# Kernel tuning notes

Measured on AMD Instinct MI355X. Metric: run time of the kernel, lower is better.

## Reference

```python
import jax, jax.numpy as jnp
import numpy as np

N = 100000
E = 1600000
IN_C = 128
OUT_C = 8
HEADS = 8
EDGE_DIM = 4
ACTUAL_OUT = OUT_C * HEADS  # 64, concat=True
BN_EPS = 1e-5
NEG_SLOPE = 0.2  # PyG GATConv default leaky_relu slope


def setup_inputs() -> dict:
    key = jax.random.key(0)
    ks = jax.random.split(key, 12)
    s = lambda fan_in: 1.0 / np.sqrt(fan_in)
    return {
        "x": jax.random.normal(ks[0], (N, IN_C), jnp.float32),
        "edge_index": jax.random.randint(ks[1], (2, E), 0, N, jnp.int64),
        "edge_attr": jax.random.normal(ks[2], (E, EDGE_DIM), jnp.float32),
        # GATConv params
        "W": jax.random.normal(ks[3], (IN_C, HEADS * OUT_C), jnp.float32) * s(IN_C),
        "att_src": jax.random.normal(ks[4], (HEADS, OUT_C), jnp.float32) * s(OUT_C),
        "att_dst": jax.random.normal(ks[5], (HEADS, OUT_C), jnp.float32) * s(OUT_C),
        "W_edge": jax.random.normal(ks[6], (EDGE_DIM, HEADS * OUT_C), jnp.float32) * s(EDGE_DIM),
        "att_edge": jax.random.normal(ks[7], (HEADS, OUT_C), jnp.float32) * s(OUT_C),
        "bias": jnp.zeros((HEADS * OUT_C,), jnp.float32),
        # BatchNorm params
        "bn_w": jnp.ones((ACTUAL_OUT,), jnp.float32),
        "bn_b": jnp.zeros((ACTUAL_OUT,), jnp.float32),
        # residual Linear (in_channels != heads*out_channels)
        "res_W": jax.random.normal(ks[8], (IN_C, ACTUAL_OUT), jnp.float32) * s(IN_C),
        "res_b": jnp.zeros((ACTUAL_OUT,), jnp.float32),
    }


def reference(x, edge_index, edge_attr, W, att_src, att_dst, W_edge, att_edge,
              bias, bn_w, bn_b, res_W, res_b):
    src, dst = edge_index[0], edge_index[1]
    n = x.shape[0]

    # --- GATConv (PyG semantics, eval mode: dropout is identity) ---
    h = (x @ W).reshape(n, HEADS, OUT_C)                       # [N,H,C]
    a_src = jnp.einsum('nhc,hc->nh', h, att_src)               # [N,H]
    a_dst = jnp.einsum('nhc,hc->nh', h, att_dst)               # [N,H]
    he = (edge_attr @ W_edge).reshape(-1, HEADS, OUT_C)        # [E,H,C]
    a_edge = jnp.einsum('ehc,hc->eh', he, att_edge)            # [E,H]

    logits = jax.nn.leaky_relu(a_src[src] + a_dst[dst] + a_edge, NEG_SLOPE)  # [E,H]
    # segment softmax over edges grouped by destination node
    m = jax.ops.segment_max(logits, dst, num_segments=n)       # [N,H]
    m = jnp.where(jnp.isfinite(m), m, 0.0)
    num = jnp.exp(logits - jax.lax.stop_gradient(m)[dst])      # [E,H]
    denom = jax.ops.segment_sum(num, dst, num_segments=n)      # [N,H]
    alpha = num / (denom[dst] + 1e-16)                         # [E,H]

    msg = alpha[:, :, None] * h[src]                           # [E,H,C]
    out = jax.ops.segment_sum(msg, dst, num_segments=n)        # [N,H,C]
    out = out.reshape(n, HEADS * OUT_C) + bias                 # concat heads

    # --- BatchNorm (training-mode batch stats, biased variance) ---
    mean = out.mean(axis=0)
    var = out.var(axis=0)
    out = (out - mean) * jax.lax.rsqrt(var + BN_EPS) * bn_w + bn_b

    # --- ELU, (dropout=identity in eval), residual ---
    out = jax.nn.elu(out)
    identity = x @ res_W + res_b
    return out + identity
```

## Files before the change

kernel.cpp:

```cpp
#include <hip/hip_runtime.h>
#include <hip/hip_bf16.h>

#define N_NODES 100000
#define N_EDGES 1600000

typedef unsigned short ushort_t;

__device__ __forceinline__ float rlane(float v, int l) {
    return __int_as_float(__builtin_amdgcn_readlane(__float_as_int(v), l));
}
__device__ __forceinline__ ushort_t f2bf(float f) {
    unsigned u = __float_as_uint(f);
    u += 0x7FFFu + ((u >> 16) & 1u);
    return (ushort_t)(u >> 16);
}
__device__ __forceinline__ float bf2f(ushort_t b) {
    return __uint_as_float((unsigned)b << 16);
}
__device__ __forceinline__ void atomic_pk_add_bf16(ushort_t* addr, unsigned packed) {
    asm volatile("global_atomic_pk_add_bf16 %0, %1, off sc1"
                 :: "v"(addr), "v"(packed) : "memory");
}

__global__ __launch_bounds__(256) void k1_node(
    const float* __restrict__ x, const float* __restrict__ W,
    const float* __restrict__ resW, const float* __restrict__ att_src,
    const float* __restrict__ att_dst, const float* __restrict__ res_b,
    ushort_t* __restrict__ h, float* __restrict__ ident,
    float* __restrict__ a_src, float* __restrict__ a_dst)
{
    __shared__ float wl[128 * 128];
    const int tid = threadIdx.x;
    for (int i = tid; i < 8192; i += 256) {
        int k = i >> 6, j = i & 63;
        wl[k * 128 + j] = W[i];
        wl[k * 128 + 64 + j] = resW[i];
    }
    __syncthreads();

    const int lane = tid & 63;
    const int wid = tid >> 6;
    const float asv = att_src[lane];
    const float adv = att_dst[lane];
    const float rbv = res_b[lane];

    for (int g = 0; g < 4; ++g) {
        const int nbase = blockIdx.x * 128 + g * 32 + wid * 8;
        float xlo[8], xhi[8], ah[8], ai[8];
        #pragma unroll
        for (int r = 0; r < 8; ++r) {
            const int n = nbase + r;
            if (n < N_NODES) {
                xlo[r] = x[(size_t)n * 128 + lane];
                xhi[r] = x[(size_t)n * 128 + 64 + lane];
            } else { xlo[r] = 0.f; xhi[r] = 0.f; }
            ah[r] = 0.f; ai[r] = 0.f;
        }
        #pragma unroll 4
        for (int k = 0; k < 64; ++k) {
            const float w0 = wl[k * 128 + lane];
            const float w1 = wl[k * 128 + 64 + lane];
            #pragma unroll
            for (int r = 0; r < 8; ++r) {
                const float xv = rlane(xlo[r], k);
                ah[r] = fmaf(w0, xv, ah[r]);
                ai[r] = fmaf(w1, xv, ai[r]);
            }
        }
        #pragma unroll 4
        for (int k = 64; k < 128; ++k) {
            const float w0 = wl[k * 128 + lane];
            const float w1 = wl[k * 128 + 64 + lane];
            #pragma unroll
            for (int r = 0; r < 8; ++r) {
                const float xv = rlane(xhi[r], k - 64);
                ah[r] = fmaf(w0, xv, ah[r]);
                ai[r] = fmaf(w1, xv, ai[r]);
            }
        }
        #pragma unroll
        for (int r = 0; r < 8; ++r) {
            const int n = nbase + r;
            float ps = ah[r] * asv;
            float pd = ah[r] * adv;
            ps += __shfl_xor(ps, 1); ps += __shfl_xor(ps, 2); ps += __shfl_xor(ps, 4);
            pd += __shfl_xor(pd, 1); pd += __shfl_xor(pd, 2); pd += __shfl_xor(pd, 4);
            if (n < N_NODES) {
                h[(size_t)n * 64 + lane] = f2bf(ah[r]);
                ident[(size_t)n * 64 + lane] = ai[r] + rbv;
                if ((lane & 7) == 0) {
                    a_src[n * 8 + (lane >> 3)] = ps;
                    a_dst[n * 8 + (lane >> 3)] = pd;
                }
            }
        }
    }
}

__global__ __launch_bounds__(256) void k2_edge(
    const int* __restrict__ ei, const float* __restrict__ ea,
    const ushort_t* __restrict__ h, const float* __restrict__ a_src,
    const float* __restrict__ a_dst, const float* __restrict__ W_edge,
    const float* __restrict__ att_edge,
    float* __restrict__ denom, ushort_t* __restrict__ out_raw)
{
    const int lane = threadIdx.x & 63;
    const int hd = lane >> 3;
    float ae0 = 0.f, ae1 = 0.f, ae2 = 0.f, ae3 = 0.f;
    #pragma unroll
    for (int c2 = 0; c2 < 8; ++c2) {
        const float a = att_edge[hd * 8 + c2];
        ae0 = fmaf(W_edge[0 * 64 + hd * 8 + c2], a, ae0);
        ae1 = fmaf(W_edge[1 * 64 + hd * 8 + c2], a, ae1);
        ae2 = fmaf(W_edge[2 * 64 + hd * 8 + c2], a, ae2);
        ae3 = fmaf(W_edge[3 * 64 + hd * 8 + c2], a, ae3);
    }

    const int gwave = blockIdx.x * 4 + (threadIdx.x >> 6);
    const int nwave = gridDim.x * 4;
    for (int base = gwave * 64; base < N_EDGES; base += nwave * 64) {
        const int vsrc = ei[base + lane];
        const int vdst = ei[N_EDGES + base + lane];
        const float4 vea = *reinterpret_cast<const float4*>(ea + (size_t)(base + lane) * 4);
        for (int g = 0; g < 64; g += 8) {
            int s[8], d[8];
            float e0[8], e1[8], e2[8], e3[8];
            #pragma unroll
            for (int j = 0; j < 8; ++j) {
                s[j] = __builtin_amdgcn_readlane(vsrc, g + j);
                d[j] = __builtin_amdgcn_readlane(vdst, g + j);
                e0[j] = rlane(vea.x, g + j);
                e1[j] = rlane(vea.y, g + j);
                e2[j] = rlane(vea.z, g + j);
                e3[j] = rlane(vea.w, g + j);
            }
            float hv[8], as8[8], ad8[8];
            #pragma unroll
            for (int j = 0; j < 8; ++j) {
                hv[j]  = bf2f(h[(size_t)s[j] * 64 + lane]);
                as8[j] = a_src[s[j] * 8 + hd];
                ad8[j] = a_dst[d[j] * 8 + hd];
            }
            #pragma unroll
            for (int j = 0; j < 8; ++j) {
                float logit = as8[j] + ad8[j]
                            + e0[j] * ae0 + e1[j] * ae1 + e2[j] * ae2 + e3[j] * ae3;
                logit = logit > 0.f ? logit : 0.2f * logit;
                const float num = __expf(logit);
                const float v = num * hv[j];
                const float vn = __shfl_xor(v, 1);
                if ((lane & 1) == 0) {
                    const unsigned packed = (unsigned)f2bf(v) | ((unsigned)f2bf(vn) << 16);
                    atomic_pk_add_bf16(out_raw + (size_t)d[j] * 64 + lane, packed);
                }
                if ((lane & 7) == 0) atomicAdd(&denom[d[j] * 8 + hd], num);
            }
        }
    }
    asm volatile("s_waitcnt vmcnt(0)" ::: "memory");
}

__global__ __launch_bounds__(256) void k3_stats(
    const ushort_t* __restrict__ out_raw, const float* __restrict__ denom,
    const float* __restrict__ bias,
    float* __restrict__ bn_acc )
{
    const int tid = threadIdx.x;
    const int c = tid & 63;
    const float b = bias[c];
    float s1 = 0.f, s2 = 0.f;
    const int stride = gridDim.x * 4;
    for (int n = blockIdx.x * 4 + (tid >> 6); n < N_NODES; n += stride) {
        const float v = bf2f(out_raw[(size_t)n * 64 + c])
                        / (denom[n * 8 + (c >> 3)] + 1e-16f) + b;
        s1 += v; s2 += v * v;
    }
    __shared__ float r1[256], r2[256];
    r1[tid] = s1; r2[tid] = s2;
    __syncthreads();
    if (tid < 64) {
        s1 = r1[tid] + r1[tid + 64] + r1[tid + 128] + r1[tid + 192];
        s2 = r2[tid] + r2[tid + 64] + r2[tid + 128] + r2[tid + 192];
        atomicAdd(&bn_acc[c], s1);
        atomicAdd(&bn_acc[64 + c], s2);
    }
}

__global__ __launch_bounds__(256) void k4_final(
    float* __restrict__ out, const ushort_t* __restrict__ out_raw,
    const float* __restrict__ denom, const float* __restrict__ bias,
    const float* __restrict__ bn_acc, const float* __restrict__ bn_w,
    const float* __restrict__ bn_b)
{
    const int tid = threadIdx.x;
    const int c = tid & 63;
    const float b = bias[c];
    const float inv_n = 1.0f / (float)N_NODES;
    const float mean = bn_acc[c] * inv_n;
    const float var = bn_acc[64 + c] * inv_n - mean * mean;
    const float sc = bn_w[c] * rsqrtf(var + 1e-5f);
    const float sh = bn_b[c] - mean * sc;
    const int stride = gridDim.x * 4;
    for (int n = blockIdx.x * 4 + (tid >> 6); n < N_NODES; n += stride) {
        float v = bf2f(out_raw[(size_t)n * 64 + c])
                  / (denom[n * 8 + (c >> 3)] + 1e-16f) + b;
        v = v * sc + sh;
        v = v > 0.f ? v : __expf(v) - 1.f;
        out[(size_t)n * 64 + c] = v + out[(size_t)n * 64 + c];
    }
}

extern "C" void kernel_launch(void* const* d_in, const int* in_sizes, int n_in,
                              void* d_out, int out_size, void* d_ws, size_t ws_size,
                              hipStream_t stream) {
    const float* x        = (const float*)d_in[0];
    const int*   ei       = (const int*)  d_in[1];
    const float* ea       = (const float*)d_in[2];
    const float* W        = (const float*)d_in[3];
    const float* att_src  = (const float*)d_in[4];
    const float* att_dst  = (const float*)d_in[5];
    const float* W_edge   = (const float*)d_in[6];
    const float* att_edge = (const float*)d_in[7];
    const float* bias     = (const float*)d_in[8];
    const float* bn_w     = (const float*)d_in[9];
    const float* bn_b     = (const float*)d_in[10];
    const float* res_W    = (const float*)d_in[11];
    const float* res_b    = (const float*)d_in[12];

    char* ws = (char*)d_ws;
    size_t off = 0;
    ushort_t* h   = (ushort_t*)(ws + off); off += (size_t)N_NODES * 64 * 2;
    float* a_src  = (float*)(ws + off); off += (size_t)N_NODES * 8 * 4;
    float* a_dst  = (float*)(ws + off); off += (size_t)N_NODES * 8 * 4;
    char*  zstart = ws + off;
    float* denom  = (float*)(ws + off); off += (size_t)N_NODES * 8 * 4;
    ushort_t* o_raw = (ushort_t*)(ws + off); off += (size_t)N_NODES * 64 * 2;
    float* bn_acc = (float*)(ws + off); off += 128 * 4;
    size_t zbytes = (size_t)((ws + off) - zstart);

    float* ident = (float*)d_out;

    (void)hipMemsetAsync(zstart, 0, zbytes, stream);
    k1_node<<<(N_NODES + 127) / 128, 256, 0, stream>>>(
        x, W, res_W, att_src, att_dst, res_b, h, ident, a_src, a_dst);
    k2_edge<<<6250, 256, 0, stream>>>(ei, ea, h, a_src, a_dst, W_edge, att_edge,
                                      denom, o_raw);
    k3_stats<<<2048, 256, 0, stream>>>(o_raw, denom, bias, bn_acc);
    k4_final<<<2048, 256, 0, stream>>>((float*)d_out, o_raw, denom, bias,
                                       bn_acc, bn_w, bn_b);
}
```

Baseline: 553.3 us.

## Compute node projection and residual GEMM with bf16 MFMA instructions

Replaces the scalar FMA/readlane node GEMM with a bf16 MFMA 16x16x32 kernel. Weight fragments are kept in registers and each wave processes 32-row tiles in a persistent grid-stride loop over 512 blocks. The aim is to shrink the time spent on the dense x@W and x@res_W products. In exchange, x and the weights are rounded to bf16, which lowers the precision of h, the attention logits and the residual identity.

Result: faster. 484.3 us (-12.5%).

```diff
diff --git a/kernel.cpp b/kernel.cpp
--- a/kernel.cpp
+++ b/kernel.cpp
@@ -5,6 +5,8 @@
 #define N_EDGES 1600000
 
 typedef unsigned short ushort_t;
+typedef __attribute__((ext_vector_type(4))) float f32x4;
+typedef __attribute__((ext_vector_type(8))) short bf16x8v;
 
 __device__ __forceinline__ float rlane(float v, int l) {
     return __int_as_float(__builtin_amdgcn_readlane(__float_as_int(v), l));
@@ -22,75 +24,98 @@
                  :: "v"(addr), "v"(packed) : "memory");
 }
 
-__global__ __launch_bounds__(256) void k1_node(
+__global__ __launch_bounds__(256) void k1_mfma(
     const float* __restrict__ x, const float* __restrict__ W,
     const float* __restrict__ resW, const float* __restrict__ att_src,
     const float* __restrict__ att_dst, const float* __restrict__ res_b,
     ushort_t* __restrict__ h, float* __restrict__ ident,
     float* __restrict__ a_src, float* __restrict__ a_dst)
 {
-    __shared__ float wl[128 * 128];
-    const int tid = threadIdx.x;
-    for (int i = tid; i < 8192; i += 256) {
-        int k = i >> 6, j = i & 63;
-        wl[k * 128 + j] = W[i];
-        wl[k * 128 + 64 + j] = resW[i];
-    }
-    __syncthreads();
-
-    const int lane = tid & 63;
-    const int wid = tid >> 6;
-    const float asv = att_src[lane];
-    const float adv = att_dst[lane];
-    const float rbv = res_b[lane];
-
-    for (int g = 0; g < 4; ++g) {
-        const int nbase = blockIdx.x * 128 + g * 32 + wid * 8;
-        float xlo[8], xhi[8], ah[8], ai[8];
-        #pragma unroll
-        for (int r = 0; r < 8; ++r) {
-            const int n = nbase + r;
-            if (n < N_NODES) {
-                xlo[r] = x[(size_t)n * 128 + lane];
-                xhi[r] = x[(size_t)n * 128 + 64 + lane];
-            } else { xlo[r] = 0.f; xhi[r] = 0.f; }
-            ah[r] = 0.f; ai[r] = 0.f;
-        }
-        #pragma unroll 4
-        for (int k = 0; k < 64; ++k) {
-            const float w0 = wl[k * 128 + lane];
-            const float w1 = wl[k * 128 + 64 + lane];
-            #pragma unroll
-            for (int r = 0; r < 8; ++r) {
-                const float xv = rlane(xlo[r], k);
-                ah[r] = fmaf(w0, xv, ah[r]);
-                ai[r] = fmaf(w1, xv, ai[r]);
-            }
-        }
-        #pragma unroll 4
-        for (int k = 64; k < 128; ++k) {
-            const float w0 = wl[k * 128 + lane];
-            const float w1 = wl[k * 128 + 64 + lane];
-            #pragma unroll
-            for (int r = 0; r < 8; ++r) {
-                const float xv = rlane(xhi[r], k - 64);
-                ah[r] = fmaf(w0, xv, ah[r]);
-                ai[r] = fmaf(w1, xv, ai[r]);
-            }
-        }
-        #pragma unroll
-        for (int r = 0; r < 8; ++r) {
-            const int n = nbase + r;
-            float ps = ah[r] * asv;
-            float pd = ah[r] * adv;
-            ps += __shfl_xor(ps, 1); ps += __shfl_xor(ps, 2); ps += __shfl_xor(ps, 4);
-            pd += __shfl_xor(pd, 1); pd += __shfl_xor(pd, 2); pd += __shfl_xor(pd, 4);
-            if (n < N_NODES) {
-                h[(size_t)n * 64 + lane] = f2bf(ah[r]);
-                ident[(size_t)n * 64 + lane] = ai[r] + rbv;
-                if ((lane & 7) == 0) {
-                    a_src[n * 8 + (lane >> 3)] = ps;
-                    a_dst[n * 8 + (lane >> 3)] = pd;
+    const int lane = threadIdx.x & 63;
+    const int col = lane & 15;
+    const int kg  = lane >> 4;
+
+    bf16x8v bfrag[4][8];
+    #pragma unroll
+    for (int ks = 0; ks < 4; ++ks) {
+        #pragma unroll
+        for (int fc = 0; fc < 8; ++fc) {
+            const int j = (fc & 3) * 16 + col;
+            const float* src = (fc < 4) ? (W + j) : (resW + j);
+            bf16x8v b;
+            #pragma unroll
+            for (int i = 0; i < 8; ++i) {
+                const int k = ks * 32 + kg * 8 + i;
+                b[i] = (short)f2bf(src[k * 64]);
+            }
+            bfrag[ks][fc] = b;
+        }
+    }
+    float atts[4], attd[4], rb[4];
+    #pragma unroll
+    for (int fc = 0; fc < 4; ++fc) {
+        atts[fc] = att_src[fc * 16 + col];
+        attd[fc] = att_dst[fc * 16 + col];
+        rb[fc]   = res_b[fc * 16 + col];
+    }
+
+    const int wid = blockIdx.x * 4 + (threadIdx.x >> 6);
+    const int nw = gridDim.x * 4;
+    for (int tile = wid; tile < 3125; tile += nw) {
+        const int row0 = tile * 32;
+        f32x4 acc[2][8];
+        #pragma unroll
+        for (int rt = 0; rt < 2; ++rt)
+            #pragma unroll
+            for (int fc = 0; fc < 8; ++fc)
+                acc[rt][fc] = (f32x4){0.f, 0.f, 0.f, 0.f};
+
+        #pragma unroll
+        for (int ks = 0; ks < 4; ++ks) {
+            bf16x8v afrag[2];
+            #pragma unroll
+            for (int rt = 0; rt < 2; ++rt) {
+                const float* xr = x + (size_t)(row0 + rt * 16 + col) * 128 + ks * 32 + kg * 8;
+                const float4 lo = *reinterpret_cast<const float4*>(xr);
+                const float4 hi = *reinterpret_cast<const float4*>(xr + 4);
+                bf16x8v a;
+                a[0] = (short)f2bf(lo.x); a[1] = (short)f2bf(lo.y);
+                a[2] = (short)f2bf(lo.z); a[3] = (short)f2bf(lo.w);
+                a[4] = (short)f2bf(hi.x); a[5] = (short)f2bf(hi.y);
+                a[6] = (short)f2bf(hi.z); a[7] = (short)f2bf(hi.w);
+                afrag[rt] = a;
+            }
+            #pragma unroll
+            for (int fc = 0; fc < 8; ++fc) {
+                acc[0][fc] = __builtin_amdgcn_mfma_f32_16x16x32_bf16(
+                    afrag[0], bfrag[ks][fc], acc[0][fc], 0, 0, 0);
+                acc[1][fc] = __builtin_amdgcn_mfma_f32_16x16x32_bf16(
+                    afrag[1], bfrag[ks][fc], acc[1][fc], 0, 0, 0);
+            }
+        }
+
+        #pragma unroll
+        for (int rt = 0; rt < 2; ++rt) {
+            #pragma unroll
+            for (int fc = 0; fc < 8; ++fc) {
+                #pragma unroll
+                for (int r = 0; r < 4; ++r) {
+                    const int row = row0 + rt * 16 + kg * 4 + r;
+                    const float val = acc[rt][fc][r];
+                    if (fc < 4) {
+                        h[(size_t)row * 64 + fc * 16 + col] = f2bf(val);
+                        float ps = val * atts[fc];
+                        float pd = val * attd[fc];
+                        ps += __shfl_xor(ps, 1); ps += __shfl_xor(ps, 2); ps += __shfl_xor(ps, 4);
+                        pd += __shfl_xor(pd, 1); pd += __shfl_xor(pd, 2); pd += __shfl_xor(pd, 4);
+                        if ((lane & 7) == 0) {
+                            const int hd = fc * 2 + (col >> 3);
+                            a_src[row * 8 + hd] = ps;
+                            a_dst[row * 8 + hd] = pd;
+                        }
+                    } else {
+                        ident[(size_t)row * 64 + (fc - 4) * 16 + col] = val + rb[fc - 4];
+                    }
                 }
             }
         }
@@ -241,7 +266,7 @@
     float* ident = (float*)d_out;
 
     (void)hipMemsetAsync(zstart, 0, zbytes, stream);
-    k1_node<<<(N_NODES + 127) / 128, 256, 0, stream>>>(
+    k1_mfma<<<512, 256, 0, stream>>>(
         x, W, res_W, att_src, att_dst, res_b, h, ident, a_src, a_dst);
     k2_edge<<<6250, 256, 0, stream>>>(ei, ea, h, a_src, a_dst, W_edge, att_edge,
                                       denom, o_raw);
```
